# Kernel optimization log

Hardware: AMD Instinct MI355X
Metric: run time of the kernel (lower is better)

Reference implementation:

```python
import jax, jax.numpy as jnp
import numpy as np

B, M = 4, 8192
NUM_PAD = 1024  # trailing pc columns zeroed to exercise the zero-column mask


def setup_inputs() -> dict:
    key = jax.random.key(0)
    k1, k2 = jax.random.split(key)
    vertices = jax.random.normal(k1, (B, 3, 128, 64), dtype=jnp.float32)
    pc = jax.random.normal(k2, (B, 3, M), dtype=jnp.float32)
    # zero-pad some columns: the original filters columns where all 3 coords == 0
    pc = pc.at[:, :, M - NUM_PAD:].set(0.0)
    return {"vertices": vertices, "pc": pc}


def reference(vertices, pc):
    b = vertices.shape[0]
    v = vertices.reshape(b, 3, -1).transpose(0, 2, 1)   # [B, N, 3] mesh vertices
    p = pc.transpose(0, 2, 1)                           # [B, M, 3] point cloud
    valid = ~jnp.all(pc == 0.0, axis=1)                 # [B, M] non-zero columns
    # squared pairwise distances pc -> vertices: [B, M, N]
    d2 = (
        jnp.sum(p * p, axis=-1)[:, :, None]
        + jnp.sum(v * v, axis=-1)[:, None, :]
        - 2.0 * jnp.einsum("bmd,bnd->bmn", p, v)
    )
    dist2 = jnp.min(d2, axis=-1)                        # [B, M] NN sq-dist per pc point
    valid_f = valid.astype(dist2.dtype)
    per_item = jnp.sum(dist2 * valid_f, axis=-1) / jnp.sum(valid_f, axis=-1)  # mean over valid points
    return jnp.mean(per_item)
```

## Files before the change

### kernel.cpp

```cpp
#include <hip/hip_runtime.h>

typedef float v2f __attribute__((ext_vector_type(2)));

#define MPTS 8192
#define NVERT 8192
#define TPB 256
#define PPT 8
#define BQ (TPB*PPT)
#define NCHUNK 32
#define VC (NVERT/NCHUNK)

__global__ __launch_bounds__(TPB) void minpart_kernel(
        const float* __restrict__ vert,
        const float* __restrict__ pc,
        float* __restrict__ partial)
{
    const int b = blockIdx.z, chunk = blockIdx.y;
    const int mbase = blockIdx.x * BQ;
    const int tid = threadIdx.x;

    const float* pcb = pc + (size_t)b * 3 * MPTS;
    v2f npx[PPT], npy[PPT], npz[PPT];
    #pragma unroll
    for (int p = 0; p < PPT; ++p) {
        const int m = mbase + p * TPB + tid;
        const float x = pcb[m], y = pcb[MPTS + m], z = pcb[2 * MPTS + m];
        npx[p] = (v2f){-2.0f * x, -2.0f * x};
        npy[p] = (v2f){-2.0f * y, -2.0f * y};
        npz[p] = (v2f){-2.0f * z, -2.0f * z};
    }

    const float* vb = vert + (size_t)b * 3 * NVERT + chunk * VC;
    const v2f* vbx = (const v2f*)(vb);
    const v2f* vby = (const v2f*)(vb + NVERT);
    const v2f* vbz = (const v2f*)(vb + 2 * NVERT);

    v2f acc[PPT];
    #pragma unroll
    for (int p = 0; p < PPT; ++p) acc[p] = (v2f){1e30f, 1e30f};

    #pragma unroll 4
    for (int j = 0; j < VC / 2; ++j) {
        const v2f vx = vbx[j], vy = vby[j], vz = vbz[j];
        const v2f vw = vx * vx + vy * vy + vz * vz;
        #pragma unroll
        for (int p = 0; p < PPT; ++p) {
            const v2f t = __builtin_elementwise_fma(npx[p], vx,
                           __builtin_elementwise_fma(npy[p], vy,
                            __builtin_elementwise_fma(npz[p], vz, vw)));
            acc[p] = __builtin_elementwise_min(acc[p], t);
        }
    }

    float* po = partial + ((size_t)b * NCHUNK + chunk) * MPTS + mbase + tid;
    #pragma unroll
    for (int p = 0; p < PPT; ++p)
        po[p * TPB] = fminf(acc[p].x, acc[p].y);
}

__global__ __launch_bounds__(256) void reduce_kernel(
        const float* __restrict__ pc,
        const float* __restrict__ partial,
        v2f* __restrict__ part)
{
    const int b = blockIdx.x >> 3, sl = blockIdx.x & 7;
    const int tid = threadIdx.x;
    const float* pcb = pc + (size_t)b * 3 * MPTS;
    const float* pb  = partial + (size_t)b * NCHUNK * MPTS;

    float sum = 0.0f, cnt = 0.0f;
    #pragma unroll
    for (int k = 0; k < 4; ++k) {
        const int m = sl * 1024 + k * 256 + tid;
        float t = pb[m];
        #pragma unroll
        for (int c = 1; c < NCHUNK; ++c)
            t = fminf(t, pb[(size_t)c * MPTS + m]);
        const float x = pcb[m], y = pcb[MPTS + m], z = pcb[2 * MPTS + m];
        const float d2 = fmaf(x, x, fmaf(y, y, fmaf(z, z, t)));
        if (!(x == 0.0f && y == 0.0f && z == 0.0f)) { sum += d2; cnt += 1.0f; }
    }
    for (int off = 32; off; off >>= 1) {
        sum += __shfl_down(sum, off);
        cnt += __shfl_down(cnt, off);
    }
    __shared__ float ss[4], sc[4];
    const int wid = tid >> 6, lane = tid & 63;
    if (lane == 0) { ss[wid] = sum; sc[wid] = cnt; }
    __syncthreads();
    if (tid == 0)
        part[blockIdx.x] = (v2f){ss[0] + ss[1] + ss[2] + ss[3],
                                 sc[0] + sc[1] + sc[2] + sc[3]};
}

__global__ __launch_bounds__(64) void final_kernel(
        const v2f* __restrict__ part, float* __restrict__ out, int B)
{
    const int lane = threadIdx.x;
    float s = 0.0f, c = 0.0f;
    if (lane < B * 8) { const v2f p = part[lane]; s = p.x; c = p.y; }
    #pragma unroll
    for (int off = 4; off; off >>= 1) {
        s += __shfl_down(s, off);
        c += __shfl_down(c, off);
    }
    const float r = s / c;
    float acc = 0.0f;
    for (int g = 0; g < B; ++g) acc += __shfl(r, g * 8);
    if (lane == 0) out[0] = acc / (float)B;
}

extern "C" void kernel_launch(void* const* d_in, const int* in_sizes, int n_in,
                              void* d_out, int out_size, void* d_ws, size_t ws_size,
                              hipStream_t stream) {
    const float* vert = (const float*)d_in[0];
    const float* pc   = (const float*)d_in[1];
    float* out        = (float*)d_out;
    const int B = in_sizes[0] / (3 * NVERT);

    float* partial = (float*)d_ws;
    v2f* part = (v2f*)(partial + (size_t)B * NCHUNK * MPTS);

    dim3 grid(MPTS / BQ, NCHUNK, B);
    minpart_kernel<<<grid, TPB, 0, stream>>>(vert, pc, partial);
    reduce_kernel<<<B * 8, 256, 0, stream>>>(pc, partial, part);
    final_kernel<<<1, 64, 0, stream>>>(part, out, B);
}
```

Baseline: 83.06 us.

## Stage vertex chunk and norms in LDS, double points per thread

Each block now loads its vertex chunk into shared memory once, stored as two float4 arrays that also carry the precomputed squared norm. The inner loop then reads two LDS vectors per vertex pair instead of three scalar-path global loads, and no longer recomputes the norm for every block. Points per thread double to 16 and vertex chunks double to 64, which keeps the grid size about the same while doubling the partial-min buffer the reduce kernel must read. The register count rises, so launch bounds ask for two blocks per CU.

Measured after the change: 128.3 us. +54.4%, slower.

```diff
diff --git a/kernel.cpp b/kernel.cpp
--- a/kernel.cpp
+++ b/kernel.cpp
@@ -5,22 +5,35 @@
 #define MPTS 8192
 #define NVERT 8192
 #define TPB 256
-#define PPT 8
+#define PPT 16
 #define BQ (TPB*PPT)
-#define NCHUNK 32
+#define NCHUNK 64
 #define VC (NVERT/NCHUNK)
+#define VPAIRS (VC/2)
 
-__global__ __launch_bounds__(TPB) void minpart_kernel(
+__global__ __launch_bounds__(TPB, 2) void minpart_kernel(
         const float* __restrict__ vert,
         const float* __restrict__ pc,
         float* __restrict__ partial)
 {
+    __shared__ float4 lvA[VPAIRS];
+    __shared__ float4 lvB[VPAIRS];
     const int b = blockIdx.z, chunk = blockIdx.y;
     const int mbase = blockIdx.x * BQ;
     const int tid = threadIdx.x;
 
+    const float* vb = vert + (size_t)b * 3 * NVERT + chunk * VC;
+    if (tid < VPAIRS) {
+        const v2f x = ((const v2f*)vb)[tid];
+        const v2f y = ((const v2f*)(vb + NVERT))[tid];
+        const v2f z = ((const v2f*)(vb + 2 * NVERT))[tid];
+        const v2f w = x * x + y * y + z * z;
+        lvA[tid] = make_float4(x.x, x.y, y.x, y.y);
+        lvB[tid] = make_float4(z.x, z.y, w.x, w.y);
+    }
+
     const float* pcb = pc + (size_t)b * 3 * MPTS;
-    v2f npx[PPT], npy[PPT], npz[PPT];
+    v2f npx[PPT], npy[PPT], npz[PPT], acc[PPT];
     #pragma unroll
     for (int p = 0; p < PPT; ++p) {
         const int m = mbase + p * TPB + tid;
@@ -28,21 +41,15 @@
         npx[p] = (v2f){-2.0f * x, -2.0f * x};
         npy[p] = (v2f){-2.0f * y, -2.0f * y};
         npz[p] = (v2f){-2.0f * z, -2.0f * z};
+        acc[p] = (v2f){1e30f, 1e30f};
     }
-
-    const float* vb = vert + (size_t)b * 3 * NVERT + chunk * VC;
-    const v2f* vbx = (const v2f*)(vb);
-    const v2f* vby = (const v2f*)(vb + NVERT);
-    const v2f* vbz = (const v2f*)(vb + 2 * NVERT);
-
-    v2f acc[PPT];
-    #pragma unroll
-    for (int p = 0; p < PPT; ++p) acc[p] = (v2f){1e30f, 1e30f};
+    __syncthreads();
 
     #pragma unroll 4
-    for (int j = 0; j < VC / 2; ++j) {
-        const v2f vx = vbx[j], vy = vby[j], vz = vbz[j];
-        const v2f vw = vx * vx + vy * vy + vz * vz;
+    for (int j = 0; j < VPAIRS; ++j) {
+        const float4 A = lvA[j], Bv = lvB[j];
+        const v2f vx = {A.x, A.y}, vy = {A.z, A.w};
+        const v2f vz = {Bv.x, Bv.y}, vw = {Bv.z, Bv.w};
         #pragma unroll
         for (int p = 0; p < PPT; ++p) {
             const v2f t = __builtin_elementwise_fma(npx[p], vx,
@@ -73,7 +80,7 @@
     for (int k = 0; k < 4; ++k) {
         const int m = sl * 1024 + k * 256 + tid;
         float t = pb[m];
-        #pragma unroll
+        #pragma unroll 8
         for (int c = 1; c < NCHUNK; ++c)
             t = fminf(t, pb[(size_t)c * MPTS + m]);
         const float x = pcb[m], y = pcb[MPTS + m], z = pcb[2 * MPTS + m];
```
